# Kernel optimization log

Hardware: AMD Instinct MI355X
Metric: run time of the kernel (lower is better)

## Reference

```python
import jax, jax.numpy as jnp
import numpy as np

N_NODES = 20000
N_EDGES = 640000
NODE_IN = 128
EDGE_IN = 64
HID = 128
OUT = 128
LOG2 = float(np.log(2.0))


def ssp(x):
    # DGL ShiftedSoftplus: softplus(x) - log(2)
    return jax.nn.softplus(x) - LOG2


def cfconv(x, e, src, dst,
           nW, nb, eW1, eb1, eW2, eb2, oW, ob):
    hv = x @ nW + nb                                  # [N, HID]
    he = ssp(ssp(e @ eW1 + eb1) @ eW2 + eb2)          # [E, HID]
    msg = hv[src] * he                                # gather + filter
    agg = jax.ops.segment_sum(msg, dst, num_segments=N_NODES)
    return ssp(agg @ oW + ob)


def setup_inputs() -> dict:
    key = jax.random.key(0)
    ks = jax.random.split(key, 20)
    def w(k, shape, fan_in):
        return jax.random.normal(k, shape, dtype=jnp.float32) * (1.0 / np.sqrt(fan_in))
    inp = {
        "node_inputs": jax.random.normal(ks[0], (N_NODES, NODE_IN), dtype=jnp.float32),
        "edge_inputs": jax.random.normal(ks[1], (N_EDGES, EDGE_IN), dtype=jnp.float32),
        "src": jax.random.randint(ks[2], (N_EDGES,), 0, N_NODES, dtype=jnp.int32),
        "dst": jax.random.randint(ks[3], (N_EDGES,), 0, N_NODES, dtype=jnp.int32),
        # conv1 params
        "n1_W": w(ks[4], (NODE_IN, HID), NODE_IN), "n1_b": jnp.zeros((HID,), jnp.float32),
        "e1_W1": w(ks[5], (EDGE_IN, HID), EDGE_IN), "e1_b1": jnp.zeros((HID,), jnp.float32),
        "e1_W2": w(ks[6], (HID, HID), HID), "e1_b2": jnp.zeros((HID,), jnp.float32),
        "o1_W": w(ks[7], (HID, HID), HID), "o1_b": jnp.zeros((HID,), jnp.float32),
        # conv2 params
        "n2_W": w(ks[8], (HID, HID), HID), "n2_b": jnp.zeros((HID,), jnp.float32),
        "e2_W1": w(ks[9], (EDGE_IN, HID), EDGE_IN), "e2_b1": jnp.zeros((HID,), jnp.float32),
        "e2_W2": w(ks[10], (HID, HID), HID), "e2_b2": jnp.zeros((HID,), jnp.float32),
        "o2_W": w(ks[11], (HID, OUT), HID), "o2_b": jnp.zeros((OUT,), jnp.float32),
    }
    return inp


def reference(node_inputs, edge_inputs, src, dst,
              n1_W, n1_b, e1_W1, e1_b1, e1_W2, e1_b2, o1_W, o1_b,
              n2_W, n2_b, e2_W1, e2_b1, e2_W2, e2_b2, o2_W, o2_b):
    h = cfconv(node_inputs, edge_inputs, src, dst,
               n1_W, n1_b, e1_W1, e1_b1, e1_W2, e1_b2, o1_W, o1_b)
    h = jnp.tanh(h)
    # dropout(p) is identity in eval mode
    h = cfconv(h, edge_inputs, src, dst,
               n2_W, n2_b, e2_W1, e2_b1, e2_W2, e2_b2, o2_W, o2_b)
    return jnp.tanh(h)
```

## Files before the change

### kernel.cpp

```cpp
#include <hip/hip_runtime.h>
#include <hip/hip_bf16.h>
#include <math.h>

typedef __bf16 bf16x8 __attribute__((ext_vector_type(8)));
typedef float f32x4 __attribute__((ext_vector_type(4)));
typedef _Float16 h16x2 __attribute__((ext_vector_type(2)));

#define LOG2F 0.6931471805599453f
#define PK1 72
#define PK2 136
#define NPB 8

__device__ __forceinline__ float sspf(float x) {
    float t = __expf(-fabsf(x));
    return fmaxf(x, 0.0f) + __logf(1.0f + t) - LOG2F;
}
__device__ __forceinline__ unsigned short f2bf(float f) {
    union { float f; unsigned u; } v; v.f = f;
    unsigned r = v.u + 0x7FFF + ((v.u >> 16) & 1);
    return (unsigned short)(r >> 16);
}
__device__ __forceinline__ float bf2f(unsigned short u) {
    union { unsigned u; float f; } v; v.u = ((unsigned)u) << 16;
    return v.f;
}
__device__ __forceinline__ unsigned short f2bf_fast(float f) {
    __bf16 h = (__bf16)f;
    return __builtin_bit_cast(unsigned short, h);
}

__global__ void convert_all(
    const float* __restrict__ A0, const float* __restrict__ A1,
    const float* __restrict__ A2, const float* __restrict__ A3,
    const float* __restrict__ A4, const float* __restrict__ A5,
    const float* __restrict__ A6, const float* __restrict__ A7,
    unsigned short* __restrict__ O0, unsigned short* __restrict__ O1,
    unsigned short* __restrict__ O2, unsigned short* __restrict__ O3,
    unsigned short* __restrict__ H4, unsigned short* __restrict__ L4,
    unsigned short* __restrict__ H5, unsigned short* __restrict__ L5,
    unsigned short* __restrict__ H6, unsigned short* __restrict__ L6,
    unsigned short* __restrict__ H7, unsigned short* __restrict__ L7)
{
    const int seg = blockIdx.x / 68;
    const int idx = (blockIdx.x % 68) * 256 + threadIdx.x;
    if (seg < 4) {
        const int PK = (seg == 0 || seg == 2) ? PK1 : PK2;
        const int K  = (seg == 0 || seg == 2) ? 64 : 128;
        if (idx >= 128 * PK) return;
        const float* W = (seg == 0) ? A0 : (seg == 1) ? A1 : (seg == 2) ? A2 : A3;
        unsigned short* O = (seg == 0) ? O0 : (seg == 1) ? O1 : (seg == 2) ? O2 : O3;
        int n = idx / PK, k = idx - n * PK;
        O[idx] = (k < K) ? f2bf(W[k * 128 + n]) : (unsigned short)0;
    } else {
        if (idx >= 128 * PK2) return;
        const float* W = (seg == 4) ? A4 : (seg == 5) ? A5 : (seg == 6) ? A6 : A7;
        unsigned short* H = (seg == 4) ? H4 : (seg == 5) ? H5 : (seg == 6) ? H6 : H7;
        unsigned short* L = (seg == 4) ? L4 : (seg == 5) ? L5 : (seg == 6) ? L6 : L7;
        int n = idx / PK2, k = idx - n * PK2;
        unsigned short h = 0, lo = 0;
        if (k < 128) {
            float w = W[k * 128 + n];
            h = f2bf(w);
            lo = f2bf(w - bf2f(h));
        }
        H[idx] = h; L[idx] = lo;
    }
}

__global__ void hist_kernel(const int* __restrict__ dst, int* __restrict__ hist, int E) {
    int i = blockIdx.x * 256 + threadIdx.x;
    if (i < E) atomicAdd(&hist[dst[i]], 1);
}
__global__ void scan_kernel(const int* __restrict__ hist, int* __restrict__ row_ptr,
                            int* __restrict__ cursor, int N) {
    __shared__ int part[1024];
    const int tid = threadIdx.x;
    const int chunk = (N + 1023) / 1024;
    const int lo = min(tid * chunk, N);
    const int hi = min(lo + chunk, N);
    int s = 0;
    for (int i = lo; i < hi; ++i) s += hist[i];
    part[tid] = s;
    __syncthreads();
    for (int d = 1; d < 1024; d <<= 1) {
        int t = (tid >= d) ? part[tid - d] : 0;
        __syncthreads();
        part[tid] += t;
        __syncthreads();
    }
    int run = part[tid] - s;
    for (int i = lo; i < hi; ++i) { row_ptr[i] = run; cursor[i] = run; run += hist[i]; }
}
__global__ void scatter_kernel(const int* __restrict__ dst, int* __restrict__ cursor,
                               int* __restrict__ perm, int E) {
    int i = blockIdx.x * 256 + threadIdx.x;
    if (i < E) { int p = atomicAdd(&cursor[dst[i]], 1); perm[p] = i; }
}
__global__ void sort_buckets(const int* __restrict__ row_ptr, const int* __restrict__ hist,
                             int* __restrict__ perm, int N) {
    int n = blockIdx.x * 256 + threadIdx.x;
    if (n >= N) return;
    const int lo = row_ptr[n], hi = lo + hist[n];
    for (int i = lo + 1; i < hi; ++i) {
        int v = perm[i]; int j = i - 1;
        while (j >= lo && perm[j] > v) { perm[j + 1] = perm[j]; --j; }
        perm[j + 1] = v;
    }
}
__global__ void permute_sd(const int* __restrict__ perm, const int* __restrict__ src,
                           const int* __restrict__ dst, int* __restrict__ srcP,
                           int* __restrict__ dstP, int E) {
    int i = blockIdx.x * 256 + threadIdx.x;
    if (i < E) { int e = perm[i]; srcP[i] = src[e]; dstP[i] = dst[e]; }
}
__global__ void permute_all(const int* __restrict__ perm, const int* __restrict__ src,
                            const int* __restrict__ dst, const float* __restrict__ Ef,
                            int* __restrict__ srcP, int* __restrict__ dstP,
                            unsigned short* __restrict__ Ebf, int nE) {
    long long idx = (long long)blockIdx.x * 256 + threadIdx.x;
    if (idx >= (long long)nE * 16) return;
    int p = (int)(idx >> 4), q = (int)(idx & 15);
    int e = perm[p];
    if (q == 0) { srcP[p] = src[e]; dstP[p] = dst[e]; }
    float4 v = *(const float4*)&Ef[(size_t)e * 64 + q * 4];
    unsigned short* o = &Ebf[(size_t)p * 64 + q * 4];
    o[0] = f2bf_fast(v.x); o[1] = f2bf_fast(v.y);
    o[2] = f2bf_fast(v.z); o[3] = f2bf_fast(v.w);
}

template<int ACT>
__global__ __launch_bounds__(256) void node_mfma3(
    const float* __restrict__ X, const unsigned short* __restrict__ WThi,
    const unsigned short* __restrict__ WTlo, const float* __restrict__ b,
    float* __restrict__ Y, int N)
{
    __shared__ unsigned short sHi[32 * PK2];
    __shared__ unsigned short sLo[32 * PK2];
    const int tid = threadIdx.x;
    const int r0 = blockIdx.x * 32;
    {
        const int r = tid >> 3, c0 = (tid & 7) * 16;
        const int row = min(r0 + r, N - 1);
        const float4* s4 = (const float4*)&X[(size_t)row * 128 + c0];
        unsigned short* dh = &sHi[r * PK2 + c0];
        unsigned short* dl = &sLo[r * PK2 + c0];
#pragma unroll
        for (int j = 0; j < 4; ++j) {
            float4 v = s4[j];
            float c[4] = { v.x, v.y, v.z, v.w };
#pragma unroll
            for (int q = 0; q < 4; ++q) {
                unsigned short h = f2bf_fast(c[q]);
                dh[j * 4 + q] = h;
                dl[j * 4 + q] = f2bf_fast(c[q] - bf2f(h));
            }
        }
    }
    __syncthreads();
    const int w = tid >> 6, l = tid & 63, cb = w * 32, lr = l & 15, hi4 = l >> 4, lk = hi4 * 8;
    const float bb[2] = { b[cb + lr], b[cb + 16 + lr] };
    f32x4 acc[2][2];
#pragma unroll
    for (int mt = 0; mt < 2; ++mt)
#pragma unroll
        for (int nt = 0; nt < 2; ++nt)
            acc[mt][nt] = (f32x4){bb[nt], bb[nt], bb[nt], bb[nt]};
    bf16x8 Bh[2][4], Bl[2][4];
#pragma unroll
    for (int nt = 0; nt < 2; ++nt)
#pragma unroll
        for (int kt = 0; kt < 4; ++kt) {
            Bh[nt][kt] = *(const bf16x8*)&WThi[(size_t)(cb + nt*16 + lr) * PK2 + kt*32 + lk];
            Bl[nt][kt] = *(const bf16x8*)&WTlo[(size_t)(cb + nt*16 + lr) * PK2 + kt*32 + lk];
        }
#pragma unroll
    for (int kt = 0; kt < 4; ++kt)
#pragma unroll
        for (int mt = 0; mt < 2; ++mt) {
            bf16x8 Ah = *(const bf16x8*)&sHi[(mt*16 + lr) * PK2 + kt*32 + lk];
            bf16x8 Al = *(const bf16x8*)&sLo[(mt*16 + lr) * PK2 + kt*32 + lk];
#pragma unroll
            for (int nt = 0; nt < 2; ++nt) {
                acc[mt][nt] = __builtin_amdgcn_mfma_f32_16x16x32_bf16(Ah, Bh[nt][kt], acc[mt][nt], 0, 0, 0);
                acc[mt][nt] = __builtin_amdgcn_mfma_f32_16x16x32_bf16(Al, Bh[nt][kt], acc[mt][nt], 0, 0, 0);
                acc[mt][nt] = __builtin_amdgcn_mfma_f32_16x16x32_bf16(Ah, Bl[nt][kt], acc[mt][nt], 0, 0, 0);
            }
        }
#pragma unroll
    for (int mt = 0; mt < 2; ++mt)
#pragma unroll
        for (int nt = 0; nt < 2; ++nt) {
            const int col = cb + nt*16 + lr;
#pragma unroll
            for (int r = 0; r < 4; ++r) {
                const int row = r0 + mt*16 + hi4*4 + r;
                if (row < N) {
                    float v = acc[mt][nt][r];
                    if (ACT) v = tanhf(sspf(v));
                    Y[(size_t)row * 128 + col] = v;
                }
            }
        }
}

__global__ __launch_bounds__(256) void node_mid(
    const float* __restrict__ AGG,
    const unsigned short* __restrict__ W1hi, const unsigned short* __restrict__ W1lo,
    const float* __restrict__ b1,
    const unsigned short* __restrict__ W2hi, const unsigned short* __restrict__ W2lo,
    const float* __restrict__ b2,
    float* __restrict__ HVout, int N)
{
    __shared__ unsigned short sHi[32 * PK2];
    __shared__ unsigned short sLo[32 * PK2];
    const int tid = threadIdx.x;
    const int r0 = blockIdx.x * 32;
    {
        const int r = tid >> 3, c0 = (tid & 7) * 16;
        const int row = min(r0 + r, N - 1);
        const float4* s4 = (const float4*)&AGG[(size_t)row * 128 + c0];
        unsigned short* dh = &sHi[r * PK2 + c0];
        unsigned short* dl = &sLo[r * PK2 + c0];
#pragma unroll
        for (int j = 0; j < 4; ++j) {
            float4 v = s4[j];
            float c[4] = { v.x, v.y, v.z, v.w };
#pragma unroll
            for (int q = 0; q < 4; ++q) {
                unsigned short h = f2bf_fast(c[q]);
                dh[j * 4 + q] = h;
                dl[j * 4 + q] = f2bf_fast(c[q] - bf2f(h));
            }
        }
    }
    __syncthreads();
    const int w = tid >> 6, l = tid & 63, cb = w * 32, lr = l & 15, hi4 = l >> 4, lk = hi4 * 8;

    f32x4 acc1[2][2];
    {
        const float bb[2] = { b1[cb + lr], b1[cb + 16 + lr] };
#pragma unroll
        for (int mt = 0; mt < 2; ++mt)
#pragma unroll
            for (int nt = 0; nt < 2; ++nt)
                acc1[mt][nt] = (f32x4){bb[nt], bb[nt], bb[nt], bb[nt]};
        bf16x8 Bh[2][4], Bl[2][4];
#pragma unroll
        for (int nt = 0; nt < 2; ++nt)
#pragma unroll
            for (int kt = 0; kt < 4; ++kt) {
                Bh[nt][kt] = *(const bf16x8*)&W1hi[(size_t)(cb + nt*16 + lr) * PK2 + kt*32 + lk];
                Bl[nt][kt] = *(const bf16x8*)&W1lo[(size_t)(cb + nt*16 + lr) * PK2 + kt*32 + lk];
            }
#pragma unroll
        for (int kt = 0; kt < 4; ++kt)
#pragma unroll
            for (int mt = 0; mt < 2; ++mt) {
                bf16x8 Ah = *(const bf16x8*)&sHi[(mt*16 + lr) * PK2 + kt*32 + lk];
                bf16x8 Al = *(const bf16x8*)&sLo[(mt*16 + lr) * PK2 + kt*32 + lk];
#pragma unroll
                for (int nt = 0; nt < 2; ++nt) {
                    acc1[mt][nt] = __builtin_amdgcn_mfma_f32_16x16x32_bf16(Ah, Bh[nt][kt], acc1[mt][nt], 0, 0, 0);
                    acc1[mt][nt] = __builtin_amdgcn_mfma_f32_16x16x32_bf16(Al, Bh[nt][kt], acc1[mt][nt], 0, 0, 0);
                    acc1[mt][nt] = __builtin_amdgcn_mfma_f32_16x16x32_bf16(Ah, Bl[nt][kt], acc1[mt][nt], 0, 0, 0);
                }
            }
    }
    __syncthreads();
#pragma unroll
    for (int mt = 0; mt < 2; ++mt)
#pragma unroll
        for (int nt = 0; nt < 2; ++nt) {
            const int col = cb + nt*16 + lr;
#pragma unroll
            for (int r = 0; r < 4; ++r) {
                const int row = mt*16 + hi4*4 + r;
                float v = tanhf(sspf(acc1[mt][nt][r]));
                unsigned short h = f2bf_fast(v);
                sHi[row * PK2 + col] = h;
                sLo[row * PK2 + col] = f2bf_fast(v - bf2f(h));
            }
        }
    __syncthreads();

    f32x4 acc2[2][2];
    {
        const float bb[2] = { b2[cb + lr], b2[cb + 16 + lr] };
#pragma unroll
        for (int mt = 0; mt < 2; ++mt)
#pragma unroll
            for (int nt = 0; nt < 2; ++nt)
                acc2[mt][nt] = (f32x4){bb[nt], bb[nt], bb[nt], bb[nt]};
        bf16x8 Bh[2][4], Bl[2][4];
#pragma unroll
        for (int nt = 0; nt < 2; ++nt)
#pragma unroll
            for (int kt = 0; kt < 4; ++kt) {
                Bh[nt][kt] = *(const bf16x8*)&W2hi[(size_t)(cb + nt*16 + lr) * PK2 + kt*32 + lk];
                Bl[nt][kt] = *(const bf16x8*)&W2lo[(size_t)(cb + nt*16 + lr) * PK2 + kt*32 + lk];
            }
#pragma unroll
        for (int kt = 0; kt < 4; ++kt)
#pragma unroll
            for (int mt = 0; mt < 2; ++mt) {
                bf16x8 Ah = *(const bf16x8*)&sHi[(mt*16 + lr) * PK2 + kt*32 + lk];
                bf16x8 Al = *(const bf16x8*)&sLo[(mt*16 + lr) * PK2 + kt*32 + lk];
#pragma unroll
                for (int nt = 0; nt < 2; ++nt) {
                    acc2[mt][nt] = __builtin_amdgcn_mfma_f32_16x16x32_bf16(Ah, Bh[nt][kt], acc2[mt][nt], 0, 0, 0);
                    acc2[mt][nt] = __builtin_amdgcn_mfma_f32_16x16x32_bf16(Al, Bh[nt][kt], acc2[mt][nt], 0, 0, 0);
                    acc2[mt][nt] = __builtin_amdgcn_mfma_f32_16x16x32_bf16(Ah, Bl[nt][kt], acc2[mt][nt], 0, 0, 0);
                }
            }
    }
#pragma unroll
    for (int mt = 0; mt < 2; ++mt)
#pragma unroll
        for (int nt = 0; nt < 2; ++nt) {
            const int col = cb + nt*16 + lr;
#pragma unroll
            for (int r = 0; r < 4; ++r) {
                const int row = r0 + mt*16 + hi4*4 + r;
                if (row < N) HVout[(size_t)row * 128 + col] = acc2[mt][nt][r];
            }
        }
}

__global__ __launch_bounds__(256) void edge_node(
    const unsigned short* __restrict__ Ebf, const int* __restrict__ srcA,
    const int* __restrict__ row_ptr, const int* __restrict__ hist,
    const float* __restrict__ HV,
    const unsigned short* __restrict__ W1T, const float* __restrict__ b1,
    const unsigned short* __restrict__ W2T, const float* __restrict__ b2,
    float* __restrict__ AGG, int N, int E)
{
    __shared__ unsigned short sT1[64 * PK2];
    __shared__ unsigned lmsg[64 * 64];
    __shared__ float lacc[NPB * 128];
    __shared__ int sSrc[64];

    const int tid = threadIdx.x;
    const int n0 = blockIdx.x * NPB;
    const int n1 = min(n0 + NPB, N);
    const int eStart = row_ptr[n0];
    const int eEnd = (n1 < N) ? row_ptr[n1] : E;

    for (int i = tid; i < NPB * 128; i += 256) lacc[i] = 0.f;

    const int w = tid >> 6, l = tid & 63, cb = w * 32, lr = l & 15, hi4 = l >> 4, lk = hi4 * 8;
    const float bb1[2] = { b1[cb + lr], b1[cb + 16 + lr] };
    const float bb2[2] = { b2[cb + lr], b2[cb + 16 + lr] };

    bf16x8 B1[2][2];
#pragma unroll
    for (int nt = 0; nt < 2; ++nt)
#pragma unroll
        for (int kt = 0; kt < 2; ++kt)
            B1[nt][kt] = *(const bf16x8*)&W1T[(size_t)(cb + nt*16 + lr) * PK1 + kt*32 + lk];
    bf16x8 B2[2][4];
#pragma unroll
    for (int nt = 0; nt < 2; ++nt)
#pragma unroll
        for (int kt = 0; kt < 4; ++kt)
            B2[nt][kt] = *(const bf16x8*)&W2T[(size_t)(cb + nt*16 + lr) * PK2 + kt*32 + lk];

    for (int t0 = eStart; t0 < eEnd; t0 += 64) {
        if (tid < 64) sSrc[tid] = srcA[min(t0 + tid, E - 1)];
        __syncthreads();

        f32x4 acc1[4][2];
#pragma unroll
        for (int mt = 0; mt < 4; ++mt)
#pragma unroll
            for (int nt = 0; nt < 2; ++nt)
                acc1[mt][nt] = (f32x4){bb1[nt], bb1[nt], bb1[nt], bb1[nt]};
#pragma unroll
        for (int kt = 0; kt < 2; ++kt)
#pragma unroll
            for (int mt = 0; mt < 4; ++mt) {
                const int row = min(t0 + mt*16 + lr, E - 1);
                bf16x8 A = *(const bf16x8*)&Ebf[(size_t)row * 64 + kt*32 + lk];
#pragma unroll
                for (int nt = 0; nt < 2; ++nt)
                    acc1[mt][nt] = __builtin_amdgcn_mfma_f32_16x16x32_bf16(A, B1[nt][kt], acc1[mt][nt], 0, 0, 0);
            }
#pragma unroll
        for (int mt = 0; mt < 4; ++mt)
#pragma unroll
            for (int nt = 0; nt < 2; ++nt) {
                const int col = cb + nt*16 + lr;
#pragma unroll
                for (int r = 0; r < 4; ++r) {
                    const int row = mt*16 + hi4*4 + r;
                    sT1[row * PK2 + col] = f2bf_fast(sspf(acc1[mt][nt][r]));
                }
            }
        __syncthreads();

        f32x4 acc2[4][2];
#pragma unroll
        for (int mt = 0; mt < 4; ++mt)
#pragma unroll
            for (int nt = 0; nt < 2; ++nt)
                acc2[mt][nt] = (f32x4){bb2[nt], bb2[nt], bb2[nt], bb2[nt]};
#pragma unroll
        for (int kt = 0; kt < 4; ++kt)
#pragma unroll
            for (int mt = 0; mt < 4; ++mt) {
                bf16x8 A = *(const bf16x8*)&sT1[(mt*16 + lr) * PK2 + kt*32 + lk];
#pragma unroll
                for (int nt = 0; nt < 2; ++nt)
                    acc2[mt][nt] = __builtin_amdgcn_mfma_f32_16x16x32_bf16(A, B2[nt][kt], acc2[mt][nt], 0, 0, 0);
            }
        const int col0 = cb + lr, col1 = cb + 16 + lr;
#pragma unroll
        for (int mt = 0; mt < 4; ++mt) {
#pragma unroll
            for (int r = 0; r < 4; ++r) {
                const int row = mt*16 + hi4*4 + r;
                const float he0 = sspf(acc2[mt][0][r]);
                const float he1 = sspf(acc2[mt][1][r]);
                const int s = sSrc[row];
                h16x2 p;
                p.x = (_Float16)(HV[(size_t)s * 128 + col0] * he0);
                p.y = (_Float16)(HV[(size_t)s * 128 + col1] * he1);
                lmsg[row * 64 + (cb >> 1) + lr] = __builtin_bit_cast(unsigned, p);
            }
        }
        __syncthreads();

        const int slot = tid & 63;
        const int cA = (slot >> 4) * 32 + (slot & 15);
        const int tEnd = min(t0 + 64, eEnd);
        for (int ln = (tid >> 6); ln < n1 - n0; ln += 4) {
            const int a0 = row_ptr[n0 + ln];
            const int a = max(a0, t0);
            const int b = min(a0 + hist[n0 + ln], tEnd);
            if (a >= b) continue;
            float f0 = 0.f, f1 = 0.f;
            for (int j = a; j < b; ++j) {
                h16x2 p = __builtin_bit_cast(h16x2, lmsg[(j - t0) * 64 + slot]);
                f0 += (float)p.x; f1 += (float)p.y;
            }
            lacc[ln * 128 + cA]      += f0;
            lacc[ln * 128 + cA + 16] += f1;
        }
        __syncthreads();
    }

    for (int i = tid; i < (n1 - n0) * 128; i += 256) {
        AGG[(size_t)(n0 + i / 128) * 128 + (i & 127)] = lacc[i];
    }
}

template<int MODE>
__global__ __launch_bounds__(256) void edge_mfma(
    const unsigned short* __restrict__ Ebf, const float* __restrict__ Ef,
    const int* __restrict__ perm,
    const int* __restrict__ srcA, const int* __restrict__ dstA,
    const float* __restrict__ HV,
    const unsigned short* __restrict__ W1T, const float* __restrict__ b1,
    const unsigned short* __restrict__ W2T, const float* __restrict__ b2,
    float* __restrict__ AGG, int nE)
{
    __shared__ unsigned short sT1[64 * PK2];
    __shared__ int sSrc[64], sDst[64];
    __shared__ unsigned short sE[(MODE == 1) ? 64 * PK1 : 4];

    const int tid = threadIdx.x;
    const int e0 = blockIdx.x * 64;

    if (tid < 64) {
        int gi = min(e0 + tid, nE - 1);
        sSrc[tid] = srcA[gi];
        sDst[tid] = dstA[gi];
    }
    if (MODE == 1) {
        const int r = tid >> 2, cc0 = (tid & 3) * 16;
        int gi = e0 + r;
        int e = (gi < nE) ? (perm ? perm[gi] : gi) : 0;
        const float4* s4 = (const float4*)&Ef[(size_t)e * 64 + cc0];
        unsigned short* dr = &sE[r * PK1 + cc0];
#pragma unroll
        for (int j = 0; j < 4; ++j) {
            float4 v = s4[j];
            dr[j*4+0] = f2bf_fast(v.x); dr[j*4+1] = f2bf_fast(v.y);
            dr[j*4+2] = f2bf_fast(v.z); dr[j*4+3] = f2bf_fast(v.w);
        }
    }
    __syncthreads();

    const int w = tid >> 6, l = tid & 63, cb = w * 32, lr = l & 15, hi4 = l >> 4, lk = hi4 * 8;
    const float bb1[2] = { b1[cb + lr], b1[cb + 16 + lr] };
    const float bb2[2] = { b2[cb + lr], b2[cb + 16 + lr] };

    bf16x8 B1[2][2];
#pragma unroll
    for (int nt = 0; nt < 2; ++nt)
#pragma unroll
        for (int kt = 0; kt < 2; ++kt)
            B1[nt][kt] = *(const bf16x8*)&W1T[(size_t)(cb + nt*16 + lr) * PK1 + kt*32 + lk];

    f32x4 acc1[4][2];
#pragma unroll
    for (int mt = 0; mt < 4; ++mt)
#pragma unroll
        for (int nt = 0; nt < 2; ++nt)
            acc1[mt][nt] = (f32x4){bb1[nt], bb1[nt], bb1[nt], bb1[nt]};
#pragma unroll
    for (int kt = 0; kt < 2; ++kt)
#pragma unroll
        for (int mt = 0; mt < 4; ++mt) {
            bf16x8 A;
            if (MODE == 0) {
                const int row = min(e0 + mt*16 + lr, nE - 1);
                A = *(const bf16x8*)&Ebf[(size_t)row * 64 + kt*32 + lk];
            } else {
                A = *(const bf16x8*)&sE[(mt*16 + lr) * PK1 + kt*32 + lk];
            }
#pragma unroll
            for (int nt = 0; nt < 2; ++nt)
                acc1[mt][nt] = __builtin_amdgcn_mfma_f32_16x16x32_bf16(A, B1[nt][kt], acc1[mt][nt], 0, 0, 0);
        }

#pragma unroll
    for (int mt = 0; mt < 4; ++mt)
#pragma unroll
        for (int nt = 0; nt < 2; ++nt) {
            const int col = cb + nt*16 + lr;
#pragma unroll
            for (int r = 0; r < 4; ++r) {
                const int row = mt*16 + hi4*4 + r;
                sT1[row * PK2 + col] = f2bf_fast(sspf(acc1[mt][nt][r]));
            }
        }
    __syncthreads();

    bf16x8 B2[2][4];
#pragma unroll
    for (int nt = 0; nt < 2; ++nt)
#pragma unroll
        for (int kt = 0; kt < 4; ++kt)
            B2[nt][kt] = *(const bf16x8*)&W2T[(size_t)(cb + nt*16 + lr) * PK2 + kt*32 + lk];

    f32x4 acc2[4][2];
#pragma unroll
    for (int mt = 0; mt < 4; ++mt)
#pragma unroll
        for (int nt = 0; nt < 2; ++nt)
            acc2[mt][nt] = (f32x4){bb2[nt], bb2[nt], bb2[nt], bb2[nt]};
#pragma unroll
    for (int kt = 0; kt < 4; ++kt)
#pragma unroll
        for (int mt = 0; mt < 4; ++mt) {
            bf16x8 A = *(const bf16x8*)&sT1[(mt*16 + lr) * PK2 + kt*32 + lk];
#pragma unroll
            for (int nt = 0; nt < 2; ++nt)
                acc2[mt][nt] = __builtin_amdgcn_mfma_f32_16x16x32_bf16(A, B2[nt][kt], acc2[mt][nt], 0, 0, 0);
        }

    const int col0 = cb + lr, col1 = cb + 16 + lr;
#pragma unroll
    for (int mt = 0; mt < 4; ++mt) {
#pragma unroll
        for (int r = 0; r < 4; ++r) {
            const int row = mt*16 + hi4*4 + r;
            if (e0 + row < nE) {
                const float he0 = sspf(acc2[mt][0][r]);
                const float he1 = sspf(acc2[mt][1][r]);
                const int s = sSrc[row], d = sDst[row];
                atomicAdd(&AGG[(size_t)d * 128 + col0], HV[(size_t)s * 128 + col0] * he0);
                atomicAdd(&AGG[(size_t)d * 128 + col1], HV[(size_t)s * 128 + col1] * he1);
            }
        }
    }
}

extern "C" void kernel_launch(void* const* d_in, const int* in_sizes, int n_in,
                              void* d_out, int out_size, void* d_ws, size_t ws_size,
                              hipStream_t stream) {
    const float* x    = (const float*)d_in[0];
    const float* e    = (const float*)d_in[1];
    const int*   src  = (const int*)  d_in[2];
    const int*   dst  = (const int*)  d_in[3];
    const float* n1W  = (const float*)d_in[4];
    const float* n1b  = (const float*)d_in[5];
    const float* e1W1 = (const float*)d_in[6];
    const float* e1b1 = (const float*)d_in[7];
    const float* e1W2 = (const float*)d_in[8];
    const float* e1b2 = (const float*)d_in[9];
    const float* o1W  = (const float*)d_in[10];
    const float* o1b  = (const float*)d_in[11];
    const float* n2W  = (const float*)d_in[12];
    const float* n2b  = (const float*)d_in[13];
    const float* e2W1 = (const float*)d_in[14];
    const float* e2b1 = (const float*)d_in[15];
    const float* e2W2 = (const float*)d_in[16];
    const float* e2b2 = (const float*)d_in[17];
    const float* o2W  = (const float*)d_in[18];
    const float* o2b  = (const float*)d_in[19];

    const int N = in_sizes[0] / 128;
    const int E = in_sizes[2];
    float* out = (float*)d_out;

    char* ws = (char*)d_ws;
    size_t off = 0;
    auto alloc = [&](size_t bytes) -> char* {
        char* p = ws + off;
        off = (off + bytes + 255) & ~(size_t)255;
        return p;
    };
    float* agg = (float*)alloc((size_t)N * 128 * 4);
    float* hv  = (float*)alloc((size_t)N * 128 * 4);
    unsigned short* w_e1w1 = (unsigned short*)alloc(128 * PK1 * 2);
    unsigned short* w_e1w2 = (unsigned short*)alloc(128 * PK2 * 2);
    unsigned short* w_e2w1 = (unsigned short*)alloc(128 * PK1 * 2);
    unsigned short* w_e2w2 = (unsigned short*)alloc(128 * PK2 * 2);
    unsigned short* n1hi = (unsigned short*)alloc(128 * PK2 * 2);
    unsigned short* n1lo = (unsigned short*)alloc(128 * PK2 * 2);
    unsigned short* o1hi = (unsigned short*)alloc(128 * PK2 * 2);
    unsigned short* o1lo = (unsigned short*)alloc(128 * PK2 * 2);
    unsigned short* n2hi = (unsigned short*)alloc(128 * PK2 * 2);
    unsigned short* n2lo = (unsigned short*)alloc(128 * PK2 * 2);
    unsigned short* o2hi = (unsigned short*)alloc(128 * PK2 * 2);
    unsigned short* o2lo = (unsigned short*)alloc(128 * PK2 * 2);
    int* perm    = (int*)alloc((size_t)E * 4);
    int* srcP    = (int*)alloc((size_t)E * 4);
    int* dstP    = (int*)alloc((size_t)E * 4);
    int* hist    = (int*)alloc((size_t)N * 4);
    int* cursor  = (int*)alloc((size_t)N * 4);
    int* row_ptr = (int*)alloc((size_t)N * 4);
    const size_t sort_need = off;
    unsigned short* Ebf = (unsigned short*)alloc((size_t)E * 64 * 2);
    const bool useEbf  = (ws_size >= off);
    const bool useSort = (ws_size >= sort_need);
    const bool useNode = useSort && useEbf;

    convert_all<<<544, 256, 0, stream>>>(
        e1W1, e1W2, e2W1, e2W2, n1W, o1W, n2W, o2W,
        w_e1w1, w_e1w2, w_e2w1, w_e2w2,
        n1hi, n1lo, o1hi, o1lo, n2hi, n2lo, o2hi, o2lo);

    const int* sA = src;
    const int* dA = dst;
    const int* permArg = nullptr;
    if (useSort) {
        hipMemsetAsync(hist, 0, (size_t)N * 4, stream);
        hist_kernel<<<(E + 255)/256, 256, 0, stream>>>(dst, hist, E);
        scan_kernel<<<1, 1024, 0, stream>>>(hist, row_ptr, cursor, N);
        scatter_kernel<<<(E + 255)/256, 256, 0, stream>>>(dst, cursor, perm, E);
        sort_buckets<<<(N + 255)/256, 256, 0, stream>>>(row_ptr, hist, perm, N);
        if (useEbf) {
            permute_all<<<(int)(((size_t)E * 16 + 255)/256), 256, 0, stream>>>(
                perm, src, dst, e, srcP, dstP, Ebf, E);
        } else {
            permute_sd<<<(E + 255)/256, 256, 0, stream>>>(perm, src, dst, srcP, dstP, E);
        }
        sA = srcP; dA = dstP; permArg = perm;
    }

    const int nodeBlocks = (N + 31) / 32;
    const int edgeNodeBlocks = (N + NPB - 1) / NPB;
    const size_t nbytes = (size_t)N * 128 * 4;

    auto run_edge_layer = [&](const unsigned short* W1T, const float* b1,
                              const unsigned short* W2T, const float* b2) {
        if (useNode) {
            edge_node<<<edgeNodeBlocks, 256, 0, stream>>>(
                Ebf, sA, row_ptr, hist, hv, W1T, b1, W2T, b2, agg, N, E);
        } else if (useEbf) {
            hipMemsetAsync(agg, 0, nbytes, stream);
            edge_mfma<0><<<(E + 63)/64, 256, 0, stream>>>(
                Ebf, nullptr, nullptr, sA, dA, hv, W1T, b1, W2T, b2, agg, E);
        } else {
            hipMemsetAsync(agg, 0, nbytes, stream);
            edge_mfma<1><<<(E + 63)/64, 256, 0, stream>>>(
                nullptr, e, permArg, sA, dA, hv, W1T, b1, W2T, b2, agg, E);
        }
    };

    node_mfma3<0><<<nodeBlocks, 256, 0, stream>>>(x, n1hi, n1lo, n1b, hv, N);
    run_edge_layer(w_e1w1, e1b1, w_e1w2, e1b2);

    node_mid<<<nodeBlocks, 256, 0, stream>>>(agg, o1hi, o1lo, o1b, n2hi, n2lo, n2b, hv, N);

    run_edge_layer(w_e2w1, e2b1, w_e2w2, e2b2);
    node_mfma3<1><<<nodeBlocks, 256, 0, stream>>>(agg, o2hi, o2lo, o2b, out, N);
}
```

Measured before the change: 760.8 us.

## Replace per-node LDS segment reduction with one-hot MFMA aggregation in edge_node

Changes the per-destination segment sum in edge_node to a matrix multiply. A one-hot bf16 matrix built from each edge's local destination index multiplies the message tile on the MFMA units. Messages are split into bf16 hi/lo pairs to keep about fp32 accuracy, and the shared-memory buffer is reused for both the intermediate tile and the transposed messages. It also doubles nodes per block to 16 to fill the 16-row MFMA output, removing the serial per-node loops and lacc scratch at the cost of extra MFMAs and a second rounding step.

```diff
diff --git a/kernel.cpp b/kernel.cpp
--- a/kernel.cpp
+++ b/kernel.cpp
@@ -4,12 +4,14 @@
 
 typedef __bf16 bf16x8 __attribute__((ext_vector_type(8)));
 typedef float f32x4 __attribute__((ext_vector_type(4)));
-typedef _Float16 h16x2 __attribute__((ext_vector_type(2)));
+typedef unsigned short u16x4 __attribute__((ext_vector_type(4)));
+typedef unsigned short u16x8 __attribute__((ext_vector_type(8)));
 
 #define LOG2F 0.6931471805599453f
 #define PK1 72
 #define PK2 136
-#define NPB 8
+#define NPB 16
+#define TPAD 72
 
 __device__ __forceinline__ float sspf(float x) {
     float t = __expf(-fabsf(x));
@@ -328,16 +330,18 @@
 
 __global__ __launch_bounds__(256) void edge_node(
     const unsigned short* __restrict__ Ebf, const int* __restrict__ srcA,
-    const int* __restrict__ row_ptr, const int* __restrict__ hist,
+    const int* __restrict__ dstA, const int* __restrict__ row_ptr,
     const float* __restrict__ HV,
     const unsigned short* __restrict__ W1T, const float* __restrict__ b1,
     const unsigned short* __restrict__ W2T, const float* __restrict__ b2,
     float* __restrict__ AGG, int N, int E)
 {
-    __shared__ unsigned short sT1[64 * PK2];
-    __shared__ unsigned lmsg[64 * 64];
-    __shared__ float lacc[NPB * 128];
-    __shared__ int sSrc[64];
+    __shared__ unsigned short sBuf[2 * 128 * TPAD];
+    __shared__ int sSrc[64], sDstLn[64];
+
+    unsigned short* sT1   = sBuf;
+    unsigned short* msgHi = sBuf;
+    unsigned short* msgLo = sBuf + 128 * TPAD;
 
     const int tid = threadIdx.x;
     const int n0 = blockIdx.x * NPB;
@@ -345,8 +349,6 @@
     const int eStart = row_ptr[n0];
     const int eEnd = (n1 < N) ? row_ptr[n1] : E;
 
-    for (int i = tid; i < NPB * 128; i += 256) lacc[i] = 0.f;
-
     const int w = tid >> 6, l = tid & 63, cb = w * 32, lr = l & 15, hi4 = l >> 4, lk = hi4 * 8;
     const float bb1[2] = { b1[cb + lr], b1[cb + 16 + lr] };
     const float bb2[2] = { b2[cb + lr], b2[cb + 16 + lr] };
@@ -364,8 +366,14 @@
         for (int kt = 0; kt < 4; ++kt)
             B2[nt][kt] = *(const bf16x8*)&W2T[(size_t)(cb + nt*16 + lr) * PK2 + kt*32 + lk];
 
+    f32x4 aggAcc[2] = {};
+
     for (int t0 = eStart; t0 < eEnd; t0 += 64) {
-        if (tid < 64) sSrc[tid] = srcA[min(t0 + tid, E - 1)];
+        if (tid < 64) {
+            const int gi = t0 + tid;
+            sSrc[tid] = srcA[min(gi, E - 1)];
+            sDstLn[tid] = (gi < eEnd) ? (dstA[gi] - n0) : -1;
+        }
         __syncthreads();
 
         f32x4 acc1[4][2];
@@ -412,44 +420,60 @@
                 for (int nt = 0; nt < 2; ++nt)
                     acc2[mt][nt] = __builtin_amdgcn_mfma_f32_16x16x32_bf16(A, B2[nt][kt], acc2[mt][nt], 0, 0, 0);
             }
-        const int col0 = cb + lr, col1 = cb + 16 + lr;
-#pragma unroll
-        for (int mt = 0; mt < 4; ++mt) {
-#pragma unroll
-            for (int r = 0; r < 4; ++r) {
-                const int row = mt*16 + hi4*4 + r;
-                const float he0 = sspf(acc2[mt][0][r]);
-                const float he1 = sspf(acc2[mt][1][r]);
-                const int s = sSrc[row];
-                h16x2 p;
-                p.x = (_Float16)(HV[(size_t)s * 128 + col0] * he0);
-                p.y = (_Float16)(HV[(size_t)s * 128 + col1] * he1);
-                lmsg[row * 64 + (cb >> 1) + lr] = __builtin_bit_cast(unsigned, p);
-            }
-        }
         __syncthreads();
 
-        const int slot = tid & 63;
-        const int cA = (slot >> 4) * 32 + (slot & 15);
-        const int tEnd = min(t0 + 64, eEnd);
-        for (int ln = (tid >> 6); ln < n1 - n0; ln += 4) {
-            const int a0 = row_ptr[n0 + ln];
-            const int a = max(a0, t0);
-            const int b = min(a0 + hist[n0 + ln], tEnd);
-            if (a >= b) continue;
-            float f0 = 0.f, f1 = 0.f;
-            for (int j = a; j < b; ++j) {
-                h16x2 p = __builtin_bit_cast(h16x2, lmsg[(j - t0) * 64 + slot]);
-                f0 += (float)p.x; f1 += (float)p.y;
-            }
-            lacc[ln * 128 + cA]      += f0;
-            lacc[ln * 128 + cA + 16] += f1;
+#pragma unroll
+        for (int nt = 0; nt < 2; ++nt) {
+            const int col = cb + nt*16 + lr;
+#pragma unroll
+            for (int mt = 0; mt < 4; ++mt) {
+                u16x4 ph, pl;
+#pragma unroll
+                for (int r = 0; r < 4; ++r) {
+                    const int row = mt*16 + hi4*4 + r;
+                    const float he = sspf(acc2[mt][nt][r]);
+                    const float m = HV[(size_t)sSrc[row] * 128 + col] * he;
+                    const unsigned short h = f2bf_fast(m);
+                    ph[r] = h;
+                    pl[r] = f2bf_fast(m - bf2f(h));
+                }
+                const int kbase = mt*16 + hi4*4;
+                *(u16x4*)&msgHi[col * TPAD + kbase] = ph;
+                *(u16x4*)&msgLo[col * TPAD + kbase] = pl;
+            }
         }
         __syncthreads();
-    }
-
-    for (int i = tid; i < (n1 - n0) * 128; i += 256) {
-        AGG[(size_t)(n0 + i / 128) * 128 + (i & 127)] = lacc[i];
+
+#pragma unroll
+        for (int kt = 0; kt < 2; ++kt) {
+            u16x8 au;
+#pragma unroll
+            for (int j = 0; j < 8; ++j) {
+                const int dn = sDstLn[kt*32 + hi4*8 + j];
+                au[j] = (dn == lr) ? (unsigned short)0x3F80 : (unsigned short)0;
+            }
+            const bf16x8 Afrag = __builtin_bit_cast(bf16x8, au);
+#pragma unroll
+            for (int nt = 0; nt < 2; ++nt) {
+                const int coff = (cb + nt*16 + lr) * TPAD + kt*32 + hi4*8;
+                bf16x8 Bh = *(const bf16x8*)&msgHi[coff];
+                bf16x8 Bl = *(const bf16x8*)&msgLo[coff];
+                aggAcc[nt] = __builtin_amdgcn_mfma_f32_16x16x32_bf16(Afrag, Bh, aggAcc[nt], 0, 0, 0);
+                aggAcc[nt] = __builtin_amdgcn_mfma_f32_16x16x32_bf16(Afrag, Bl, aggAcc[nt], 0, 0, 0);
+            }
+        }
+        __syncthreads();
+    }
+
+#pragma unroll
+    for (int nt = 0; nt < 2; ++nt) {
+        const int col = cb + nt*16 + lr;
+#pragma unroll
+        for (int r = 0; r < 4; ++r) {
+            const int row = hi4*4 + r;
+            if (n0 + row < n1)
+                AGG[(size_t)(n0 + row) * 128 + col] = aggAcc[nt][r];
+        }
     }
 }
 
@@ -668,7 +692,7 @@
                               const unsigned short* W2T, const float* b2) {
         if (useNode) {
             edge_node<<<edgeNodeBlocks, 256, 0, stream>>>(
-                Ebf, sA, row_ptr, hist, hv, W1T, b1, W2T, b2, agg, N, E);
+                Ebf, sA, dA, row_ptr, hv, W1T, b1, W2T, b2, agg, N, E);
         } else if (useEbf) {
             hipMemsetAsync(agg, 0, nbytes, stream);
             edge_mfma<0><<<(E + 63)/64, 256, 0, stream>>>(
```

After: 684.1 us. -10.1%, faster.
